# Kernel tuning notes

Measured on AMD Instinct MI355X. Metric: run time of the kernel, lower is better.

Reference implementation:

```python
import jax, jax.numpy as jnp
import numpy as np

DIM = 1024
HEADS = 16
DIM_HEAD = DIM // HEADS
SCALE = DIM_HEAD ** -0.5


def setup_inputs() -> dict:
    key = jax.random.key(0)
    k1, k2, k3 = jax.random.split(key, 3)
    x = jax.random.normal(k1, (4, 2048, DIM), dtype=jnp.float32)
    # q_lin: Linear(dim, 3*dim, bias=False); store as [dim, 3*dim] for x @ W
    w_qkv = jax.random.normal(k2, (DIM, 3 * DIM), dtype=jnp.float32) * (DIM ** -0.5)
    w_out = jax.random.normal(k3, (DIM, DIM), dtype=jnp.float32) * (DIM ** -0.5)
    return {"x": x, "w_qkv": w_qkv, "w_out": w_out}


def reference(x, w_qkv, w_out):
    b, n, d = x.shape
    qkv = x @ w_qkv  # [b, n, 3d]
    q, k, v = jnp.split(qkv, 3, axis=-1)
    # b n (h d) -> b h n d
    def to_heads(t):
        return t.reshape(b, n, HEADS, DIM_HEAD).transpose(0, 2, 1, 3)
    q, k, v = to_heads(q), to_heads(k), to_heads(v)
    sim = jnp.einsum('bhnj,bhmj->bhnm', q, k) * SCALE
    causal = jnp.triu(jnp.ones((n, n), dtype=bool), k=1)
    sim = jnp.where(causal, -jnp.finfo(sim.dtype).max, sim)
    attn = jax.nn.softmax(sim, axis=-1)
    out = jnp.einsum('bhnm,bhmd->bhnd', attn, v)
    out = out.transpose(0, 2, 1, 3).reshape(b, n, d)  # b h n d -> b n (h d)
    return out @ w_out
```

## Files before the change

kernel.cpp:

```cpp
#include <hip/hip_runtime.h>
#include <hip/hip_bf16.h>
#include <stdint.h>

#define SEQ  2048
#define DIMM 1024
#define NH   16
#define DH   64
#define NB   4
#define MROWS (NB*SEQ)
#define QKP  2080

typedef __attribute__((ext_vector_type(8))) short bf16x8;
typedef __attribute__((ext_vector_type(4))) float f32x4;
typedef __attribute__((ext_vector_type(16))) float f32x16;

#define LOG2E 1.44269504088896340736f

template<bool B> struct BoolC { static constexpr bool value = B; };

__device__ __forceinline__ unsigned short f2bf(float f) {
    union { float f; uint32_t u; } c; c.f = f;
    uint32_t r = c.u + 0x7fff + ((c.u >> 16) & 1);
    return (unsigned short)(r >> 16);
}

__device__ __forceinline__ void gload_lds16(const void* g, void* lds) {
    __builtin_amdgcn_global_load_lds(
        (const __attribute__((address_space(1))) unsigned int*)(g),
        (__attribute__((address_space(3))) unsigned int*)(lds),
        16, 0, 0);
}

__global__ __launch_bounds__(256) void k_prep(const float* __restrict__ x,
                                              unsigned short* __restrict__ x_bf,
                                              const float* __restrict__ w_qkv,
                                              unsigned short* __restrict__ wqkvT,
                                              const float* __restrict__ w_out,
                                              unsigned short* __restrict__ woutT) {
    __shared__ unsigned short tile[32][33];
    const int bid = blockIdx.x;
    if (bid < 8192) {
        int i = bid * 256 + threadIdx.x;
        float4 v = ((const float4*)x)[i];
        ushort4 o;
        o.x = f2bf(v.x); o.y = f2bf(v.y); o.z = f2bf(v.z); o.w = f2bf(v.w);
        ((ushort4*)x_bf)[i] = o;
        return;
    }
    const float* W;
    unsigned short* Wt;
    int tn, tk, N;
    if (bid < 8192 + 3072) {
        W = w_qkv; Wt = wqkvT; N = 3072;
        tn = (bid - 8192) % 96; tk = (bid - 8192) / 96;
    } else {
        W = w_out; Wt = woutT; N = 1024;
        tn = (bid - 11264) % 32; tk = (bid - 11264) / 32;
    }
    const int K = 1024;
    int lx = threadIdx.x & 31, ly = threadIdx.x >> 5;
    #pragma unroll
    for (int i = 0; i < 32; i += 8) {
        int k = tk * 32 + ly + i;
        int n = tn * 32 + lx;
        tile[ly + i][lx] = f2bf(W[(size_t)k * N + n]);
    }
    __syncthreads();
    int k2 = tk * 32 + lx;
    #pragma unroll
    for (int i = 0; i < 32; i += 8) {
        int n2 = tn * 32 + ly + i;
        Wt[(size_t)n2 * K + k2] = tile[lx][ly + i];
    }
}

template<int MODE>
__global__ __launch_bounds__(256) void k_gemm_bt(const unsigned short* __restrict__ A,
                                                 const unsigned short* __restrict__ Bt,
                                                 void* __restrict__ Cv,
                                                 unsigned short* __restrict__ vtv,
                                                 int M, int N_, int K) {
    constexpr int BM = 128, BN = 128, BK = 64;
    __shared__ unsigned short lA[BM * BK];
    __shared__ unsigned short lB[BN * BK];
    const int ntile = N_ / BN;
    const int wgid = (blockIdx.x & 7) * (gridDim.x >> 3) + (blockIdx.x >> 3);
    const int tm = wgid / ntile;
    const int tn = wgid % ntile;
    const int t = threadIdx.x;
    const int w = t >> 6, l = t & 63;
    const int wr = w >> 1, wc = w & 1;

    const unsigned short* Abase = A + (size_t)tm * BM * K;
    const unsigned short* Bbase = Bt + (size_t)tn * BN * K;

    f32x4 acc[4][4] = {};

    const int rswz = (l & 7) << 4;

    for (int k0 = 0; k0 < K; k0 += BK) {
        __syncthreads();
        #pragma unroll
        for (int i = 0; i < 4; ++i) {
            const int o  = i * 4096 + t * 16;
            const int so = o ^ (((o >> 7) & 7) << 4);
            const int row = so >> 7;
            const int kb  = so & 127;
            gload_lds16((const char*)(Abase + (size_t)row * K + k0) + kb,
                        (char*)lA + i * 4096 + w * 1024);
            gload_lds16((const char*)(Bbase + (size_t)row * K + k0) + kb,
                        (char*)lB + i * 4096 + w * 1024);
        }
        __syncthreads();

        #pragma unroll
        for (int kk = 0; kk < 2; ++kk) {
            bf16x8 af[4], bfv[4];
            #pragma unroll
            for (int i = 0; i < 4; ++i) {
                const int ea = ((wr * 64 + i * 16 + (l & 15)) << 7) + kk * 64 + ((l >> 4) << 4);
                af[i] = *(const bf16x8*)((const char*)lA + (ea ^ rswz));
            }
            #pragma unroll
            for (int j = 0; j < 4; ++j) {
                const int eb = ((wc * 64 + j * 16 + (l & 15)) << 7) + kk * 64 + ((l >> 4) << 4);
                bfv[j] = *(const bf16x8*)((const char*)lB + (eb ^ rswz));
            }
            #pragma unroll
            for (int i = 0; i < 4; ++i)
                #pragma unroll
                for (int j = 0; j < 4; ++j)
                    acc[i][j] = __builtin_amdgcn_mfma_f32_16x16x32_bf16(af[i], bfv[j], acc[i][j], 0, 0, 0);
        }
    }

    const int row0 = tm * BM + wr * 64 + (l >> 4) * 4;
    const int col0 = tn * BN + wc * 64 + (l & 15);

    if (MODE == 0) {
        float* Cf = (float*)Cv;
        #pragma unroll
        for (int i = 0; i < 4; ++i)
            #pragma unroll
            for (int j = 0; j < 4; ++j)
                #pragma unroll
                for (int r = 0; r < 4; ++r)
                    Cf[(size_t)(row0 + i * 16 + r) * N_ + (col0 + j * 16)] = acc[i][j][r];
    } else if (tn < 16) {
        const float cs = (tn < 8) ? 0.125f * LOG2E : 1.0f;
        unsigned short* qk = (unsigned short*)Cv;
        #pragma unroll
        for (int i = 0; i < 4; ++i)
            #pragma unroll
            for (int j = 0; j < 4; ++j)
                #pragma unroll
                for (int r = 0; r < 4; ++r)
                    qk[(size_t)(row0 + i * 16 + r) * QKP + (col0 + j * 16)] = f2bf(acc[i][j][r] * cs);
    } else {
        #pragma unroll
        for (int i = 0; i < 4; ++i) {
            const int rbase = row0 + i * 16;
            const int bq = rbase >> 11;
            const int n0 = rbase & 2047;
            #pragma unroll
            for (int j = 0; j < 4; ++j) {
                const int c = col0 + j * 16 - 2048;
                const int hh = c >> 6, dd = c & 63;
                uint2 u;
                u.x = (unsigned int)f2bf(acc[i][j][0]) | ((unsigned int)f2bf(acc[i][j][1]) << 16);
                u.y = (unsigned int)f2bf(acc[i][j][2]) | ((unsigned int)f2bf(acc[i][j][3]) << 16);
                *(uint2*)(vtv + ((size_t)(bq * 16 + hh) * 64 + dd) * QKP + n0) = u;
            }
        }
    }
}

__global__ __launch_bounds__(256, 2) void k_attn20(const unsigned short* __restrict__ qk,
                                                   const unsigned short* __restrict__ vt,
                                                   unsigned short* __restrict__ out) {
    const int bid = blockIdx.x;
    const int bh = bid & 63;
    const int w = threadIdx.x >> 6;
    const int c32 = 63 - ((bid >> 6) * 4 + w);
    const int b = bh >> 4, h = bh & 15;
    const int l = threadIdx.x & 63;
    const int l31 = l & 31, hi = l >> 5;

    const unsigned short* qp = qk + (size_t)(b * SEQ) * QKP + h * 64;
    unsigned short* op = out + (size_t)(b * SEQ) * DIMM + h * 64;

    constexpr int KSTEP = 64 * QKP * 2;
    constexpr int VSTEP = 64 * 2;

    union U8 { uint32_t u[4]; bf16x8 v; };

    const int q0w = c32 * 32;
    const int qrow = q0w + l31;
    const int nt = (q0w >> 6) + 1;

    bf16x8 qf[4];
    #pragma unroll
    for (int m = 0; m < 4; ++m)
        qf[m] = *(const bf16x8*)(qp + (size_t)(q0w + l31) * QKP + m * 16 + hi * 8);

    f32x16 accO0 = {}, accO1 = {};
    float m_run = -INFINITY, l_run = 0.f;

    const char* kp0 = (const char*)(qk + ((size_t)b * SEQ + l31) * QKP + 1024 + h * 64 + hi * 8);
    const char* kp1 = kp0 + 32 * QKP * 2;
    const char* vp0 = (const char*)(vt + ((size_t)bh * 64 + l31) * QKP + hi * 8);
    const char* vp1 = vp0 + 32 * QKP * 2;

    bf16x8 kf[2][4];
    #pragma unroll
    for (int m = 0; m < 4; ++m) {
        kf[0][m] = *(const bf16x8*)(kp0 + m * 32);
        kf[1][m] = *(const bf16x8*)(kp1 + m * 32);
    }
    kp0 += KSTEP; kp1 += KSTEP;

    auto tile = [&](int kv0, auto mskc) {
        constexpr bool MSK = decltype(mskc)::value;

        f32x16 s0 = {}, s1 = {};
        __builtin_amdgcn_s_setprio(1);
        #pragma unroll
        for (int m = 0; m < 4; ++m) {
            s0 = __builtin_amdgcn_mfma_f32_32x32x16_bf16(kf[0][m], qf[m], s0, 0, 0, 0);
            s1 = __builtin_amdgcn_mfma_f32_32x32x16_bf16(kf[1][m], qf[m], s1, 0, 0, 0);
        }
        __builtin_amdgcn_s_setprio(0);

        bf16x8 vf0[4], vf1[4];
        #pragma unroll
        for (int m = 0; m < 4; ++m) {
            vf0[m] = *(const bf16x8*)(vp0 + m * 32);
            vf1[m] = *(const bf16x8*)(vp1 + m * 32);
        }
        vp0 += VSTEP; vp1 += VSTEP;

        #pragma unroll
        for (int m = 0; m < 4; ++m) {
            kf[0][m] = *(const bf16x8*)(kp0 + m * 32);
            kf[1][m] = *(const bf16x8*)(kp1 + m * 32);
        }
        kp0 += KSTEP; kp1 += KSTEP;

        float tmax = -1e30f;
        #pragma unroll
        for (int r = 0; r < 16; ++r) {
            float v0 = s0[r];
            float v1 = s1[r];
            if (MSK) {
                const int crow = (r & 3) + 8 * (r >> 2) + 4 * hi;
                if (kv0 + crow > qrow)      v0 = -1e30f;
                if (kv0 + 32 + crow > qrow) v1 = -1e30f;
                s0[r] = v0; s1[r] = v1;
            }
            tmax = fmaxf(tmax, fmaxf(v0, v1));
        }
        tmax = fmaxf(tmax, __shfl_xor(tmax, 32));
        const bool defer = __all(tmax <= m_run + 8.0f);
        float fct = 1.0f;
        if (!defer) {
            const float mnew = fmaxf(m_run, tmax);
            fct = exp2f(m_run - mnew);
            m_run = mnew;
            #pragma unroll
            for (int r = 0; r < 16; ++r) { accO0[r] *= fct; accO1[r] *= fct; }
        }
        float ps = 0.f;
        #pragma unroll
        for (int r = 0; r < 16; ++r) {
            float p0 = exp2f(s0[r] - m_run);
            float p1 = exp2f(s1[r] - m_run);
            s0[r] = p0; s1[r] = p1;
            ps += p0 + p1;
        }
        ps += __shfl_xor(ps, 32);
        l_run = l_run * fct + ps;

        uint32_t pw0[8], pw1[8];
        #pragma unroll
        for (int i = 0; i < 8; ++i) {
            asm("v_cvt_pk_bf16_f32 %0, %1, %2" : "=v"(pw0[i]) : "v"(s0[2*i]), "v"(s0[2*i+1]));
            asm("v_cvt_pk_bf16_f32 %0, %1, %2" : "=v"(pw1[i]) : "v"(s1[2*i]), "v"(s1[2*i+1]));
        }
        __builtin_amdgcn_s_setprio(1);
        #define PVCHUNK(PW, BASE, VF0, VF1) do {                                     \
            uint32_t a0 = PW[BASE+0], b0 = PW[BASE+2];                               \
            uint32_t a1 = PW[BASE+1], b1 = PW[BASE+3];                               \
            asm("v_permlane32_swap_b32 %0, %1" : "+v"(a0), "+v"(b0));                \
            asm("v_permlane32_swap_b32 %0, %1" : "+v"(a1), "+v"(b1));                \
            U8 pb; pb.u[0] = a0; pb.u[1] = a1; pb.u[2] = b0; pb.u[3] = b1;           \
            accO0 = __builtin_amdgcn_mfma_f32_32x32x16_bf16(VF0, pb.v, accO0, 0, 0, 0); \
            accO1 = __builtin_amdgcn_mfma_f32_32x32x16_bf16(VF1, pb.v, accO1, 0, 0, 0); \
        } while (0)
        PVCHUNK(pw0, 0, vf0[0], vf1[0]);
        PVCHUNK(pw0, 4, vf0[1], vf1[1]);
        PVCHUNK(pw1, 0, vf0[2], vf1[2]);
        PVCHUNK(pw1, 4, vf0[3], vf1[3]);
        #undef PVCHUNK
        __builtin_amdgcn_s_setprio(0);
    };

    for (int kt = 0; kt + 1 < nt; ++kt) tile(kt * 64, BoolC<false>{});
    tile((nt - 1) * 64, BoolC<true>{});

    const float inv = 1.0f / l_run;
    unsigned short* orow = op + (size_t)(q0w + l31) * DIMM;
    #pragma unroll
    for (int g = 0; g < 4; ++g) {
        uint2 u0, u1;
        float a0 = accO0[4*g+0] * inv, a1 = accO0[4*g+1] * inv;
        float a2 = accO0[4*g+2] * inv, a3 = accO0[4*g+3] * inv;
        float c0 = accO1[4*g+0] * inv, c1 = accO1[4*g+1] * inv;
        float c2 = accO1[4*g+2] * inv, c3 = accO1[4*g+3] * inv;
        asm("v_cvt_pk_bf16_f32 %0, %1, %2" : "=v"(u0.x) : "v"(a0), "v"(a1));
        asm("v_cvt_pk_bf16_f32 %0, %1, %2" : "=v"(u0.y) : "v"(a2), "v"(a3));
        asm("v_cvt_pk_bf16_f32 %0, %1, %2" : "=v"(u1.x) : "v"(c0), "v"(c1));
        asm("v_cvt_pk_bf16_f32 %0, %1, %2" : "=v"(u1.y) : "v"(c2), "v"(c3));
        *(uint2*)(orow + 8*g + 4*hi)      = u0;
        *(uint2*)(orow + 32 + 8*g + 4*hi) = u1;
    }
}

extern "C" void kernel_launch(void* const* d_in, const int* in_sizes, int n_in,
                              void* d_out, int out_size, void* d_ws, size_t ws_size,
                              hipStream_t stream) {
    const float* x     = (const float*)d_in[0];
    const float* w_qkv = (const float*)d_in[1];
    const float* w_out = (const float*)d_in[2];

    unsigned short* x_bf   = (unsigned short*)d_ws;
    unsigned short* wqkvT  = x_bf   + (size_t)MROWS * DIMM;
    unsigned short* woutT  = wqkvT  + (size_t)3 * DIMM * DIMM;
    unsigned short* qk_buf = woutT  + (size_t)DIMM * DIMM;
    unsigned short* vt     = qk_buf + (size_t)MROWS * QKP;
    unsigned short* aout   = vt     + (size_t)64 * DH * QKP;

    k_prep<<<8192 + 3072 + 1024, 256, 0, stream>>>(x, x_bf, w_qkv, wqkvT, w_out, woutT);

    k_gemm_bt<1><<<(MROWS / 128) * (3 * DIMM / 128), 256, 0, stream>>>(
        x_bf, wqkvT, qk_buf, vt, MROWS, 3 * DIMM, DIMM);

    k_attn20<<<1024, 256, 0, stream>>>(qk_buf, vt, aout);

    k_gemm_bt<0><<<(MROWS / 128) * (DIMM / 128), 256, 0, stream>>>(
        aout, woutT, d_out, nullptr, MROWS, DIMM, DIMM);
}
```

Measured before the change: 198.1 us.

## Replace QKV projection GEMM with double-buffered 128x256 tile kernel using 8 waves

Adds a dedicated QKV GEMM kernel with 512 threads, a 128x256 output tile and double-buffered LDS. It prefetches the next K-slice with async global-to-LDS loads while MFMAs run, and raises wave priority around MFMA blocks. The aim is to hide global load latency and get more reuse per tile than the single-buffered 128x128 kernel. The generic GEMM is reduced to the fp32-output path. The change uses more LDS (96KB) and allows one block per CU.

```diff
diff --git a/kernel.cpp b/kernel.cpp
--- a/kernel.cpp
+++ b/kernel.cpp
@@ -74,11 +74,139 @@
     }
 }
 
-template<int MODE>
+__global__ __launch_bounds__(512, 1) void k_gemm8(const unsigned short* __restrict__ A,
+                                                  const unsigned short* __restrict__ Bt,
+                                                  unsigned short* __restrict__ qkv_q,
+                                                  unsigned short* __restrict__ vtv) {
+    __shared__ unsigned short lA[2][128 * 64];
+    __shared__ unsigned short lB[2][256 * 64];
+    const int ntile = 12;
+    const int wgid = (blockIdx.x & 7) * 96 + (blockIdx.x >> 3);
+    const int tm = wgid / ntile;
+    const int tn = wgid % ntile;
+    const int t = threadIdx.x;
+    const int w = t >> 6, l = t & 63;
+    const int wr = w >> 2, wc = w & 3;
+
+    const unsigned short* Abase = A + (size_t)tm * 128 * 1024;
+    const unsigned short* Bbase = Bt + (size_t)tn * 256 * 1024;
+
+    f32x4 acc[4][4] = {};
+    const int rswz = (l & 7) << 4;
+
+    auto STAGE = [&](int ks, int bs) {
+        const int k0 = ks * 64;
+        #pragma unroll
+        for (int i = 0; i < 2; ++i) {
+            const int o  = i * 8192 + t * 16;
+            const int so = o ^ (((o >> 7) & 7) << 4);
+            gload_lds16((const char*)(Abase + (size_t)(so >> 7) * 1024 + k0) + (so & 127),
+                        (char*)lA[bs] + i * 8192 + w * 1024);
+        }
+        #pragma unroll
+        for (int i = 0; i < 4; ++i) {
+            const int o  = i * 8192 + t * 16;
+            const int so = o ^ (((o >> 7) & 7) << 4);
+            gload_lds16((const char*)(Bbase + (size_t)(so >> 7) * 1024 + k0) + (so & 127),
+                        (char*)lB[bs] + i * 8192 + w * 1024);
+        }
+    };
+
+    STAGE(0, 0);
+    STAGE(1, 1);
+    asm volatile("s_waitcnt vmcnt(6)" ::: "memory");
+    __builtin_amdgcn_s_barrier();
+
+    for (int ks = 0; ks < 16; ++ks) {
+        const char* la = (const char*)lA[ks & 1];
+        const char* lb = (const char*)lB[ks & 1];
+        bf16x8 af[2][2], bfv[4][2];
+
+        #pragma unroll
+        for (int m = 0; m < 2; ++m)
+            #pragma unroll
+            for (int kk = 0; kk < 2; ++kk) {
+                const int ea = ((wr * 64 + m * 16 + (l & 15)) << 7) + kk * 64 + ((l >> 4) << 4);
+                af[m][kk] = *(const bf16x8*)(la + (ea ^ rswz));
+            }
+        #pragma unroll
+        for (int n = 0; n < 4; ++n)
+            #pragma unroll
+            for (int kk = 0; kk < 2; ++kk) {
+                const int eb = ((wc * 64 + n * 16 + (l & 15)) << 7) + kk * 64 + ((l >> 4) << 4);
+                bfv[n][kk] = *(const bf16x8*)(lb + (eb ^ rswz));
+            }
+        __builtin_amdgcn_s_setprio(1);
+        #pragma unroll
+        for (int m = 0; m < 2; ++m)
+            #pragma unroll
+            for (int n = 0; n < 4; ++n)
+                #pragma unroll
+                for (int kk = 0; kk < 2; ++kk)
+                    acc[m][n] = __builtin_amdgcn_mfma_f32_16x16x32_bf16(af[m][kk], bfv[n][kk], acc[m][n], 0, 0, 0);
+        __builtin_amdgcn_s_setprio(0);
+
+        #pragma unroll
+        for (int m = 0; m < 2; ++m)
+            #pragma unroll
+            for (int kk = 0; kk < 2; ++kk) {
+                const int ea = ((wr * 64 + (m + 2) * 16 + (l & 15)) << 7) + kk * 64 + ((l >> 4) << 4);
+                af[m][kk] = *(const bf16x8*)(la + (ea ^ rswz));
+            }
+        __builtin_amdgcn_sched_barrier(0);
+        __builtin_amdgcn_s_barrier();
+
+        if (ks < 15) STAGE(ks + 2 < 16 ? ks + 2 : 15, ks & 1);
+
+        __builtin_amdgcn_s_setprio(1);
+        #pragma unroll
+        for (int m = 0; m < 2; ++m)
+            #pragma unroll
+            for (int n = 0; n < 4; ++n)
+                #pragma unroll
+                for (int kk = 0; kk < 2; ++kk)
+                    acc[m + 2][n] = __builtin_amdgcn_mfma_f32_16x16x32_bf16(af[m][kk], bfv[n][kk], acc[m + 2][n], 0, 0, 0);
+        __builtin_amdgcn_s_setprio(0);
+
+        if (ks < 15) {
+            asm volatile("s_waitcnt vmcnt(6)" ::: "memory");
+            __builtin_amdgcn_s_barrier();
+        }
+    }
+
+    const int row0 = tm * 128 + wr * 64 + (l >> 4) * 4;
+    const int col0 = tn * 256 + wc * 64 + (l & 15);
+    if (tn < 8) {
+        const float cs = (tn < 4) ? 0.125f * LOG2E : 1.0f;
+        #pragma unroll
+        for (int i = 0; i < 4; ++i)
+            #pragma unroll
+            for (int j = 0; j < 4; ++j)
+                #pragma unroll
+                for (int r = 0; r < 4; ++r)
+                    qkv_q[(size_t)(row0 + i * 16 + r) * QKP + (col0 + j * 16)] = f2bf(acc[i][j][r] * cs);
+    } else {
+        #pragma unroll
+        for (int i = 0; i < 4; ++i) {
+            const int rbase = row0 + i * 16;
+            const int bq = rbase >> 11;
+            const int n0 = rbase & 2047;
+            #pragma unroll
+            for (int j = 0; j < 4; ++j) {
+                const int c = col0 + j * 16 - 2048;
+                const int hh = c >> 6, dd = c & 63;
+                uint2 u;
+                u.x = (unsigned int)f2bf(acc[i][j][0]) | ((unsigned int)f2bf(acc[i][j][1]) << 16);
+                u.y = (unsigned int)f2bf(acc[i][j][2]) | ((unsigned int)f2bf(acc[i][j][3]) << 16);
+                *(uint2*)(vtv + ((size_t)(bq * 16 + hh) * 64 + dd) * QKP + n0) = u;
+            }
+        }
+    }
+}
+
 __global__ __launch_bounds__(256) void k_gemm_bt(const unsigned short* __restrict__ A,
                                                  const unsigned short* __restrict__ Bt,
-                                                 void* __restrict__ Cv,
-                                                 unsigned short* __restrict__ vtv,
+                                                 float* __restrict__ Cf,
                                                  int M, int N_, int K) {
     constexpr int BM = 128, BN = 128, BK = 64;
     __shared__ unsigned short lA[BM * BK];
@@ -95,7 +223,6 @@
     const unsigned short* Bbase = Bt + (size_t)tn * BN * K;
 
     f32x4 acc[4][4] = {};
-
     const int rswz = (l & 7) << 4;
 
     for (int k0 = 0; k0 < K; k0 += BK) {
@@ -104,11 +231,9 @@
         for (int i = 0; i < 4; ++i) {
             const int o  = i * 4096 + t * 16;
             const int so = o ^ (((o >> 7) & 7) << 4);
-            const int row = so >> 7;
-            const int kb  = so & 127;
-            gload_lds16((const char*)(Abase + (size_t)row * K + k0) + kb,
+            gload_lds16((const char*)(Abase + (size_t)(so >> 7) * K + k0) + (so & 127),
                         (char*)lA + i * 4096 + w * 1024);
-            gload_lds16((const char*)(Bbase + (size_t)row * K + k0) + kb,
+            gload_lds16((const char*)(Bbase + (size_t)(so >> 7) * K + k0) + (so & 127),
                         (char*)lB + i * 4096 + w * 1024);
         }
         __syncthreads();
@@ -136,46 +261,16 @@
 
     const int row0 = tm * BM + wr * 64 + (l >> 4) * 4;
     const int col0 = tn * BN + wc * 64 + (l & 15);
-
-    if (MODE == 0) {
-        float* Cf = (float*)Cv;
-        #pragma unroll
-        for (int i = 0; i < 4; ++i)
-            #pragma unroll
-            for (int j = 0; j < 4; ++j)
-                #pragma unroll
-                for (int r = 0; r < 4; ++r)
-                    Cf[(size_t)(row0 + i * 16 + r) * N_ + (col0 + j * 16)] = acc[i][j][r];
-    } else if (tn < 16) {
-        const float cs = (tn < 8) ? 0.125f * LOG2E : 1.0f;
-        unsigned short* qk = (unsigned short*)Cv;
-        #pragma unroll
-        for (int i = 0; i < 4; ++i)
-            #pragma unroll
-            for (int j = 0; j < 4; ++j)
-                #pragma unroll
-                for (int r = 0; r < 4; ++r)
-                    qk[(size_t)(row0 + i * 16 + r) * QKP + (col0 + j * 16)] = f2bf(acc[i][j][r] * cs);
-    } else {
-        #pragma unroll
-        for (int i = 0; i < 4; ++i) {
-            const int rbase = row0 + i * 16;
-            const int bq = rbase >> 11;
-            const int n0 = rbase & 2047;
-            #pragma unroll
-            for (int j = 0; j < 4; ++j) {
-                const int c = col0 + j * 16 - 2048;
-                const int hh = c >> 6, dd = c & 63;
-                uint2 u;
-                u.x = (unsigned int)f2bf(acc[i][j][0]) | ((unsigned int)f2bf(acc[i][j][1]) << 16);
-                u.y = (unsigned int)f2bf(acc[i][j][2]) | ((unsigned int)f2bf(acc[i][j][3]) << 16);
-                *(uint2*)(vtv + ((size_t)(bq * 16 + hh) * 64 + dd) * QKP + n0) = u;
-            }
-        }
-    }
-}
-
-__global__ __launch_bounds__(256, 2) void k_attn20(const unsigned short* __restrict__ qk,
+    #pragma unroll
+    for (int i = 0; i < 4; ++i)
+        #pragma unroll
+        for (int j = 0; j < 4; ++j)
+            #pragma unroll
+            for (int r = 0; r < 4; ++r)
+                Cf[(size_t)(row0 + i * 16 + r) * N_ + (col0 + j * 16)] = acc[i][j][r];
+}
+
+__global__ __launch_bounds__(256, 2) void k_attn21(const unsigned short* __restrict__ qk,
                                                    const unsigned short* __restrict__ vt,
                                                    unsigned short* __restrict__ out) {
     const int bid = blockIdx.x;
@@ -341,11 +436,10 @@
 
     k_prep<<<8192 + 3072 + 1024, 256, 0, stream>>>(x, x_bf, w_qkv, wqkvT, w_out, woutT);
 
-    k_gemm_bt<1><<<(MROWS / 128) * (3 * DIMM / 128), 256, 0, stream>>>(
-        x_bf, wqkvT, qk_buf, vt, MROWS, 3 * DIMM, DIMM);
-
-    k_attn20<<<1024, 256, 0, stream>>>(qk_buf, vt, aout);
-
-    k_gemm_bt<0><<<(MROWS / 128) * (DIMM / 128), 256, 0, stream>>>(
-        aout, woutT, d_out, nullptr, MROWS, DIMM, DIMM);
-}
+    k_gemm8<<<768, 512, 0, stream>>>(x_bf, wqkvT, qk_buf, vt);
+
+    k_attn21<<<1024, 256, 0, stream>>>(qk_buf, vt, aout);
+
+    k_gemm_bt<<<(MROWS / 128) * (DIMM / 128), 256, 0, stream>>>(
+        aout, woutT, (float*)d_out, MROWS, DIMM, DIMM);
+}
```

After: 201.5 us. No clear change (+1.7%).
